# Kernel tuning notes

Measured on AMD Instinct MI355X. Metric: run time of the kernel, lower is better.

The kernel has to match this reference:

```python
import jax, jax.numpy as jnp
import numpy as np

KNN_K = 5  # nearest neighbors for local density
PATCH_GRID = 14  # hard-coded p1=p2=14 in rearrange


def _tokens(x):
    # b c (p1 h) (p2 w) -> b (p1 p2) (h w c)
    B, C, H, W = x.shape
    P = PATCH_GRID
    h, w = H // P, W // P
    t = x.reshape(B, C, P, h, P, w).transpose(0, 2, 4, 3, 5, 1)
    return t.reshape(B, P * P, h * w * C)


def _forward(x, len_keep):
    t = _tokens(x)
    B, N, Cf = t.shape
    # pairwise Euclidean distance (torch.cdist) scaled by sqrt(C)
    sq = jnp.sum(t * t, axis=-1)  # [B, N]
    d2 = sq[:, :, None] + sq[:, None, :] - 2.0 * jnp.einsum('bnc,bmc->bnm', t, t)
    dist = jnp.sqrt(jnp.maximum(d2, 0.0)) / jnp.sqrt(jnp.asarray(Cf, dist_dtype := t.dtype))
    # k-NN local density
    neg_vals, _ = jax.lax.top_k(-dist, KNN_K)  # k smallest distances
    dist_nearest = -neg_vals  # [B, N, k]
    density = jnp.exp(-jnp.mean(dist_nearest ** 2, axis=-1))  # [B, N]
    kd = jax.random.fold_in(jax.random.key(1), 0)
    density = density + jax.random.uniform(kd, density.shape, dtype=density.dtype) * 1e-6
    # distance to nearest higher-density point (masked min reduction)
    maskf = (density[:, None, :] > density[:, :, None]).astype(dist.dtype)  # [B, N, N]
    dist_max = jnp.max(dist.reshape(B, -1), axis=-1)[:, None, None]
    dmin = jnp.min(dist * maskf + dist_max * (1.0 - maskf), axis=-1)  # [B, N]
    score = dmin * density
    # pick cluster centers: top len_keep scores
    _, index_down = jax.lax.top_k(score, len_keep)  # [B, K]
    # assign each token to nearest center
    dm_down = jnp.take_along_axis(dist, index_down[:, :, None], axis=1)  # [B, K, N]
    idx_cluster = jnp.argmin(dm_down, axis=1)  # [B, N]
    # force centers to their own cluster id
    idx_cluster = idx_cluster.at[jnp.arange(B)[:, None], index_down].set(
        jnp.arange(len_keep)[None, :])
    # per-cluster counts (every cluster id 0..K-1 present since centers self-assign)
    counts = jnp.sum(jax.nn.one_hot(idx_cluster, len_keep, dtype=jnp.int32), axis=1)  # [B, K]
    idx_counts = jnp.cumsum(counts, axis=-1)
    # pick one representative token per cluster via noisy sort
    kn = jax.random.fold_in(jax.random.key(1), 1)
    noise = jax.random.uniform(kn, (B, N), dtype=dist.dtype)
    order = jnp.argsort(idx_cluster.astype(dist.dtype) + noise, axis=-1)
    idx = jnp.take_along_axis(order, idx_counts - 1, axis=1)  # [B, K]
    return idx


def setup_inputs() -> dict:
    key = jax.random.key(0)
    x = jax.random.normal(key, (256, 3, 224, 224), dtype=jnp.float32)
    return {"x": x, "len_keep": 49}


def reference(x, len_keep):
    return _forward(x, len_keep)
```

## Files before the change

### kernel.cpp

```cpp
#include <hip/hip_runtime.h>
#include <stdint.h>

#define NTOK 196
#define KCL 49
#define IMG 224
#define IMG2 (224*224)
#define KB 64
#define LDP 68

typedef double f64x4 __attribute__((ext_vector_type(4)));

__host__ __device__ __forceinline__ void tf2x32(uint32_t k0, uint32_t k1,
    uint32_t x0, uint32_t x1, uint32_t* o0, uint32_t* o1) {
  uint32_t ks2 = k0 ^ k1 ^ 0x1BD11BDAu;
#define TFR(r) { x0 += x1; x1 = (x1 << r) | (x1 >> (32 - r)); x1 ^= x0; }
  x0 += k0; x1 += k1;
  TFR(13) TFR(15) TFR(26) TFR(6)
  x0 += k1; x1 += ks2 + 1u;
  TFR(17) TFR(29) TFR(16) TFR(24)
  x0 += ks2; x1 += k0 + 2u;
  TFR(13) TFR(15) TFR(26) TFR(6)
  x0 += k0; x1 += k1 + 3u;
  TFR(17) TFR(29) TFR(16) TFR(24)
  x0 += k1; x1 += ks2 + 4u;
  TFR(13) TFR(15) TFR(26) TFR(6)
  x0 += ks2; x1 += k0 + 5u;
#undef TFR
  *o0 = x0; *o1 = x1;
}

__device__ __forceinline__ float jax_uniform(uint32_t k0, uint32_t k1, uint32_t j) {
  uint32_t o0, o1;
  tf2x32(k0, k1, 0u, j, &o0, &o1);
  uint32_t bits = o0 ^ o1;
  return __uint_as_float((bits >> 9) | 0x3f800000u) - 1.0f;
}

__global__ void __launch_bounds__(256) k_sq(const float* __restrict__ x,
                                            double* __restrict__ sq, int B) {
  int wave = blockIdx.x * 4 + (threadIdx.x >> 6);
  int lane = threadIdx.x & 63;
  if (wave >= B * NTOK) return;
  int b = wave / NTOK, n = wave % NTOK;
  int p1 = n / 14, p2 = n % 14;
  const float* xb = x + (size_t)b * 3 * IMG2;
  int rowbase = (p1 * 16) * IMG + p2 * 16;
  double acc = 0.0;
#pragma unroll
  for (int q = 0; q < 12; ++q) {
    int f = lane + q * 64;
    int c = f >> 8, h = (f >> 4) & 15, w = f & 15;
    float v = xb[c * IMG2 + rowbase + h * IMG + w];
    acc += (double)v * (double)v;
  }
#pragma unroll
  for (int off = 32; off; off >>= 1) acc += __shfl_down(acc, off);
  if (lane == 0) sq[wave] = acc;
}

__global__ void __launch_bounds__(256) k_dist_mfma(const float* __restrict__ x,
    const double* __restrict__ sq, double* __restrict__ dist,
    unsigned long long* __restrict__ dmax) {
  int bid = blockIdx.x;
  int xcd = bid & 7;
  int s = bid >> 3;
  int b = xcd + 8 * (s / 28);
  int t = s % 28;
  int ti = 0, rem = t, rl = 7;
  while (rem >= rl) { rem -= rl; rl--; ti++; }
  int tj = ti + rem;
  int n0b = ti * 32, m0b = tj * 32;
  int tid = threadIdx.x;

  __shared__ __align__(16) float As[32][LDP];
  __shared__ __align__(16) float Bs[32][LDP];
  __shared__ int rbN[32], rbM[32];
  __shared__ double prsh[3];
  __shared__ int okf;

  if (tid < 32) {
    int n = n0b + tid; n = n < NTOK ? n : NTOK - 1;
    rbN[tid] = (n / 14) * 16 * IMG + (n % 14) * 16;
  } else if (tid < 64) {
    int m = m0b + (tid - 32); m = m < NTOK ? m : NTOK - 1;
    rbM[tid - 32] = (m / 14) * 16 * IMG + (m % 14) * 16;
  }
  __syncthreads();

  const float* xb = x + (size_t)b * 3 * IMG2;
  int srow = tid >> 3;
  int sfo  = (tid & 7) * 8;
  int rN = rbN[srow], rM = rbM[srow];
  int lane = tid & 63;
  int wid  = tid >> 6;
  int wi = wid >> 1, wj = wid & 1;
  int aq = lane >> 4;
  const float* Ap = &As[0][0];
  const float* Bp = &Bs[0][0];
  int abase = (wi * 16 + (lane & 15)) * LDP + aq;
  int bbase = (wj * 16 + (lane & 15)) * LDP + aq;

#define LOADT(d0,d1,d2,d3,kc) { int f0 = (kc) + sfo;                         \
    int c_ = f0 >> 8, h_ = (f0 >> 4) & 15, w_ = f0 & 15;                     \
    const float* p_ = xb + c_ * IMG2 + h_ * IMG + w_;                        \
    d0 = *(const float4*)(p_ + rN); d1 = *(const float4*)(p_ + rN + 4);      \
    d2 = *(const float4*)(p_ + rM); d3 = *(const float4*)(p_ + rM + 4); }

  f64x4 acc = {0.0, 0.0, 0.0, 0.0};
  f64x4 acc0 = {0.0, 0.0, 0.0, 0.0};
  float4 ca0, ca1, cb0, cb1;
  LOADT(ca0, ca1, cb0, cb1, 0)

#pragma unroll
  for (int tt = 0; tt < 12; ++tt) {
    __syncthreads();
    *(float4*)&As[srow][sfo]     = ca0;
    *(float4*)&As[srow][sfo + 4] = ca1;
    *(float4*)&Bs[srow][sfo]     = cb0;
    *(float4*)&Bs[srow][sfo + 4] = cb1;
    __syncthreads();
    float4 na0, na1, nb0, nb1;
    if (tt < 11) LOADT(na0, na1, nb0, nb1, (tt + 1) * KB)
#pragma unroll
    for (int k = 0; k < KB; k += 4) {
      double av = (double)Ap[abase + k];
      double bv = (double)Bp[bbase + k];
      acc = __builtin_amdgcn_mfma_f64_16x16x4f64(av, bv, acc, 0, 0, 0);
    }
    if (tt == 0) {
      if (wid == 0) {
        double q0 = (double)As[0][lane] * (double)Bs[0][lane];
        double q1 = (double)As[1][lane] * (double)Bs[0][lane];
        double q2 = (double)As[4][lane] * (double)Bs[0][lane];
#pragma unroll
        for (int off = 32; off; off >>= 1) {
          q0 += __shfl_down(q0, off);
          q1 += __shfl_down(q1, off);
          q2 += __shfl_down(q2, off);
        }
        if (lane == 0) { prsh[0] = q0; prsh[1] = q1; prsh[2] = q2; }
      }
      acc0 = acc;
    }
    ca0 = na0; ca1 = na1; cb0 = nb0; cb1 = nb1;
  }
#undef LOADT

  if (tid == 0) {
    double tol = 1e-9 * (1.0 + fabs(prsh[0]));
    int ok0  = fabs(prsh[0] - acc0[0]) <= tol;
    int okP1 = ok0 && (fabs(prsh[1] - acc0[1]) <= tol);
    int okP2 = ok0 && (fabs(prsh[2] - acc0[1]) <= tol);
    okf = okP1 ? 1 : (okP2 ? 2 : 0);
  }
  __syncthreads();
  int mode = okf;

  double (*Dt)[33] = (double(*)[33])(&As[0][0]);

  if (mode) {
#pragma unroll
    for (int i = 0; i < 4; ++i) {
      int lr = (mode == 1) ? (aq * 4 + i) : (aq + 4 * i);
      Dt[wi * 16 + lr][wj * 16 + (lane & 15)] = acc[i];
    }
  } else {
    double s00 = 0, s01 = 0, s10 = 0, s11 = 0;
    int ty2 = tid >> 4, tx2 = tid & 15;
    for (int kc = 0; kc < 768; kc += KB) {
      int f0 = kc + sfo;
      int c_ = f0 >> 8, h_ = (f0 >> 4) & 15, w_ = f0 & 15;
      const float* p_ = xb + c_ * IMG2 + h_ * IMG + w_;
      float4 la0 = *(const float4*)(p_ + rN), la1 = *(const float4*)(p_ + rN + 4);
      float4 lb0 = *(const float4*)(p_ + rM), lb1 = *(const float4*)(p_ + rM + 4);
      __syncthreads();
      *(float4*)&As[srow][sfo]     = la0;
      *(float4*)&As[srow][sfo + 4] = la1;
      *(float4*)&Bs[srow][sfo]     = lb0;
      *(float4*)&Bs[srow][sfo + 4] = lb1;
      __syncthreads();
      for (int j = 0; j < KB; ++j) {
        double a0 = (double)As[ty2][j], a1 = (double)As[ty2 + 16][j];
        double b0 = (double)Bs[tx2][j], b1 = (double)Bs[tx2 + 16][j];
        s00 += a0 * b0; s01 += a0 * b1; s10 += a1 * b0; s11 += a1 * b1;
      }
    }
    __syncthreads();
    Dt[ty2][tx2] = s00;       Dt[ty2][tx2 + 16] = s01;
    Dt[ty2 + 16][tx2] = s10;  Dt[ty2 + 16][tx2 + 16] = s11;
  }
  __syncthreads();

  const double* sqb = sq + b * NTOK;
  const double SQ768 = sqrt(768.0);
  int lr2 = tid >> 3, lc0 = (tid & 7) * 4;
  double dv[4];
  double lmax = 0.0;
#pragma unroll
  for (int j = 0; j < 4; ++j) {
    int n = n0b + lr2, m = m0b + lc0 + j;
    int nn = n < NTOK ? n : NTOK - 1, mm = m < NTOK ? m : NTOK - 1;
    double d2 = sqb[nn] + sqb[mm] - 2.0 * Dt[lr2][lc0 + j];
    double d = sqrt(d2 > 0.0 ? d2 : 0.0) / SQ768;
    dv[j] = d;
    Dt[lr2][lc0 + j] = d;
    lmax = lmax > d ? lmax : d;
  }
  double* red = (double*)(&Bs[0][0]);
  red[tid] = lmax;
  __syncthreads();
  for (int st = 128; st; st >>= 1) {
    if (tid < st) { double o = red[tid + st]; if (o > red[tid]) red[tid] = o; }
    __syncthreads();
  }
  if (tid == 0) atomicMax(&dmax[b], (unsigned long long)__double_as_longlong(red[0]));

  double* Db = dist + (size_t)b * NTOK * NTOK;
  {
    int n = n0b + lr2, m0 = m0b + lc0;
    if (n < NTOK && m0 < NTOK) {
      if (m0 + 3 < NTOK) {
        f64x4 v = {dv[0], dv[1], dv[2], dv[3]};
        *(f64x4*)(Db + (size_t)n * NTOK + m0) = v;
      } else {
#pragma unroll
        for (int j = 0; j < 4; ++j)
          if (m0 + j < NTOK) Db[(size_t)n * NTOK + m0 + j] = dv[j];
      }
    }
  }
  if (ti != tj) {
    int m = m0b + lr2, n0 = n0b + lc0;
    if (m < NTOK && n0 < NTOK) {
      if (n0 + 3 < NTOK) {
        f64x4 v = {Dt[lc0][lr2], Dt[lc0 + 1][lr2], Dt[lc0 + 2][lr2], Dt[lc0 + 3][lr2]};
        *(f64x4*)(Db + (size_t)m * NTOK + n0) = v;
      } else {
#pragma unroll
        for (int j = 0; j < 4; ++j)
          if (n0 + j < NTOK) Db[(size_t)m * NTOK + n0 + j] = Dt[lc0 + j][lr2];
      }
    }
  }
}

__global__ void __launch_bounds__(256) k_cluster(const double* __restrict__ dist,
    const unsigned long long* __restrict__ dmax, int* __restrict__ out,
    uint32_t kd0, uint32_t kd1, uint32_t kn0, uint32_t kn1, int B) {
  int b = blockIdx.x;
  int tid = threadIdx.x;
  int lane = tid & 63, wid = tid >> 6;
  const double* Db = dist + (size_t)b * NTOK * NTOK;
  __shared__ double dens[NTOK];
  __shared__ double score[NTOK];
  __shared__ int center[KCL];
  __shared__ short center_of[NTOK];
  __shared__ unsigned long long bkey[KCL];
  double dmaxv = __longlong_as_double((long long)dmax[b]);

  if (tid < NTOK) {
    double nb0 = 1e300, nb1 = 1e300, nb2 = 1e300, nb3 = 1e300, nb4 = 1e300;
    for (int m = 0; m < NTOK; ++m) {
      double v = Db[(size_t)m * NTOK + tid];
      if (v < nb4) {
        nb4 = v;
        if (nb4 < nb3) { double t = nb3; nb3 = nb4; nb4 = t;
          if (nb3 < nb2) { t = nb2; nb2 = nb3; nb3 = t;
            if (nb2 < nb1) { t = nb1; nb1 = nb2; nb2 = t;
              if (nb1 < nb0) { t = nb0; nb0 = nb1; nb1 = t; } } } }
      }
    }
    double acc = nb0 * nb0 + nb1 * nb1 + nb2 * nb2 + nb3 * nb3 + nb4 * nb4;
    double mean = acc / 5.0;
    double d = exp(-mean);
    double u = (double)jax_uniform(kd0, kd1, (uint32_t)(b * NTOK + tid));
    dens[tid] = d + u * 1e-6;
  }
  __syncthreads();

  if (tid < NTOK) {
    double dn = dens[tid];
    double v = dmaxv;
    for (int m = 0; m < NTOK; ++m) {
      double r = Db[(size_t)m * NTOK + tid];
      if (dens[m] > dn && r < v) v = r;
    }
    score[tid] = v * dn;
  }
  __syncthreads();

  if (wid == 0) {
    double s0 = (lane < NTOK) ? score[lane] : -1e300;
    double s1 = score[lane + 64];
    double s2 = score[lane + 128];
    double s3 = (lane + 192 < NTOK) ? score[lane + 192] : -1e300;
    for (int k = 0; k < KCL; ++k) {
      double mv = s0; int mi = lane;
      if (s1 > mv) { mv = s1; mi = lane + 64; }
      if (s2 > mv) { mv = s2; mi = lane + 128; }
      if (s3 > mv) { mv = s3; mi = lane + 192; }
#pragma unroll
      for (int off = 32; off; off >>= 1) {
        double ov = __shfl_down(mv, off); int oi = __shfl_down(mi, off);
        if (ov > mv || (ov == mv && oi < mi)) { mv = ov; mi = oi; }
      }
      mi = __shfl(mi, 0);
      if (lane == 0) center[k] = mi;
      if (mi == lane) s0 = -1e300;
      else if (mi == lane + 64) s1 = -1e300;
      else if (mi == lane + 128) s2 = -1e300;
      else if (mi == lane + 192) s3 = -1e300;
    }
  }
  __syncthreads();

  if (tid < NTOK) center_of[tid] = -1;
  __syncthreads();
  if (tid < KCL) { center_of[center[tid]] = (short)tid; bkey[tid] = 0ULL; }
  __syncthreads();
  int mycl = 0;
  if (tid < NTOK) {
    double best = 1e300; int bk = 0;
    for (int k = 0; k < KCL; ++k) {
      double d = Db[(size_t)center[k] * NTOK + tid];
      if (d < best) { best = d; bk = k; }
    }
    short co = center_of[tid];
    if (co >= 0) bk = co;
    mycl = bk;
  }
  __syncthreads();

  if (tid < NTOK) {
    float u = jax_uniform(kn0, kn1, (uint32_t)(b * NTOK + tid));
    float keyf = (float)mycl + u;
    unsigned long long key =
        ((unsigned long long)__float_as_uint(keyf) << 8) | (unsigned)tid;
    atomicMax(&bkey[mycl], key);
  }
  __syncthreads();
  if (tid < KCL) out[b * KCL + tid] = (int)(bkey[tid] & 0xFFu);
}

extern "C" void kernel_launch(void* const* d_in, const int* in_sizes, int n_in,
                              void* d_out, int out_size, void* d_ws, size_t ws_size,
                              hipStream_t stream) {
  const float* x = (const float*)d_in[0];
  int B = in_sizes[0] / (3 * IMG2);
  double* dist = (double*)d_ws;
  size_t distBytes = (size_t)B * NTOK * NTOK * sizeof(double);
  double* sq = (double*)((char*)d_ws + distBytes);
  unsigned long long* dmax =
      (unsigned long long*)((char*)sq + (size_t)B * NTOK * sizeof(double));
  int* out = (int*)d_out;

  uint32_t kd0, kd1, kn0, kn1;
  tf2x32(0u, 1u, 0u, 0u, &kd0, &kd1);
  tf2x32(0u, 1u, 0u, 1u, &kn0, &kn1);

  hipMemsetAsync(dmax, 0, B * sizeof(unsigned long long), stream);
  int totalTok = B * NTOK;
  k_sq<<<dim3((totalTok + 3) / 4), dim3(256), 0, stream>>>(x, sq, B);
  k_dist_mfma<<<dim3(8 * 32 * 28), dim3(256), 0, stream>>>(x, sq, dist, dmax);
  k_cluster<<<dim3(B), dim3(256), 0, stream>>>(dist, dmax, out, kd0, kd1, kn0, kn1, B);
}
```

Before: 364.2 us.

## Fuse squared-norm computation into distance kernel and split cluster scans across 512 threads

Removes the separate k_sq kernel by accumulating per-token squared norms inside the distance kernel from the tiles it already loads, then reducing them in shared memory. This saves one launch and a re-read of the input, at the cost of extra FP64 FMAs and shared memory in the distance kernel. The cluster kernel now uses 512 threads, and each token's kNN and masked-min column scans are split into two halves that are merged through shared memory. This doubles parallelism over the per-batch serial dependency chain.

```diff
diff --git a/kernel.cpp b/kernel.cpp
--- a/kernel.cpp
+++ b/kernel.cpp
@@ -36,31 +36,8 @@
   return __uint_as_float((bits >> 9) | 0x3f800000u) - 1.0f;
 }
 
-__global__ void __launch_bounds__(256) k_sq(const float* __restrict__ x,
-                                            double* __restrict__ sq, int B) {
-  int wave = blockIdx.x * 4 + (threadIdx.x >> 6);
-  int lane = threadIdx.x & 63;
-  if (wave >= B * NTOK) return;
-  int b = wave / NTOK, n = wave % NTOK;
-  int p1 = n / 14, p2 = n % 14;
-  const float* xb = x + (size_t)b * 3 * IMG2;
-  int rowbase = (p1 * 16) * IMG + p2 * 16;
-  double acc = 0.0;
-#pragma unroll
-  for (int q = 0; q < 12; ++q) {
-    int f = lane + q * 64;
-    int c = f >> 8, h = (f >> 4) & 15, w = f & 15;
-    float v = xb[c * IMG2 + rowbase + h * IMG + w];
-    acc += (double)v * (double)v;
-  }
-#pragma unroll
-  for (int off = 32; off; off >>= 1) acc += __shfl_down(acc, off);
-  if (lane == 0) sq[wave] = acc;
-}
-
 __global__ void __launch_bounds__(256) k_dist_mfma(const float* __restrict__ x,
-    const double* __restrict__ sq, double* __restrict__ dist,
-    unsigned long long* __restrict__ dmax) {
+    double* __restrict__ dist, unsigned long long* __restrict__ dmax) {
   int bid = blockIdx.x;
   int xcd = bid & 7;
   int s = bid >> 3;
@@ -77,6 +54,8 @@
   __shared__ int rbN[32], rbM[32];
   __shared__ double prsh[3];
   __shared__ int okf;
+  __shared__ double sqpA[32][8], sqpB[32][8];
+  __shared__ double sqN[32], sqM[32];
 
   if (tid < 32) {
     int n = n0b + tid; n = n < NTOK ? n : NTOK - 1;
@@ -108,6 +87,7 @@
 
   f64x4 acc = {0.0, 0.0, 0.0, 0.0};
   f64x4 acc0 = {0.0, 0.0, 0.0, 0.0};
+  double psqA = 0.0, psqB = 0.0;
   float4 ca0, ca1, cb0, cb1;
   LOADT(ca0, ca1, cb0, cb1, 0)
 
@@ -118,6 +98,14 @@
     *(float4*)&As[srow][sfo + 4] = ca1;
     *(float4*)&Bs[srow][sfo]     = cb0;
     *(float4*)&Bs[srow][sfo + 4] = cb1;
+    psqA += (double)ca0.x * ca0.x; psqA += (double)ca0.y * ca0.y;
+    psqA += (double)ca0.z * ca0.z; psqA += (double)ca0.w * ca0.w;
+    psqA += (double)ca1.x * ca1.x; psqA += (double)ca1.y * ca1.y;
+    psqA += (double)ca1.z * ca1.z; psqA += (double)ca1.w * ca1.w;
+    psqB += (double)cb0.x * cb0.x; psqB += (double)cb0.y * cb0.y;
+    psqB += (double)cb0.z * cb0.z; psqB += (double)cb0.w * cb0.w;
+    psqB += (double)cb1.x * cb1.x; psqB += (double)cb1.y * cb1.y;
+    psqB += (double)cb1.z * cb1.z; psqB += (double)cb1.w * cb1.w;
     __syncthreads();
     float4 na0, na1, nb0, nb1;
     if (tt < 11) LOADT(na0, na1, nb0, nb1, (tt + 1) * KB)
@@ -146,6 +134,8 @@
   }
 #undef LOADT
 
+  sqpA[srow][tid & 7] = psqA;
+  sqpB[srow][tid & 7] = psqB;
   if (tid == 0) {
     double tol = 1e-9 * (1.0 + fabs(prsh[0]));
     int ok0  = fabs(prsh[0] - acc0[0]) <= tol;
@@ -189,23 +179,32 @@
     Dt[ty2][tx2] = s00;       Dt[ty2][tx2 + 16] = s01;
     Dt[ty2 + 16][tx2] = s10;  Dt[ty2 + 16][tx2 + 16] = s11;
   }
-  __syncthreads();
-
-  const double* sqb = sq + b * NTOK;
+  if (tid < 32) {
+    double a = sqpA[tid][0];
+#pragma unroll
+    for (int j = 1; j < 8; ++j) a += sqpA[tid][j];
+    sqN[tid] = a;
+  } else if (tid < 64) {
+    double a = sqpB[tid - 32][0];
+#pragma unroll
+    for (int j = 1; j < 8; ++j) a += sqpB[tid - 32][j];
+    sqM[tid - 32] = a;
+  }
+  __syncthreads();
+
   const double SQ768 = sqrt(768.0);
   int lr2 = tid >> 3, lc0 = (tid & 7) * 4;
   double dv[4];
   double lmax = 0.0;
 #pragma unroll
   for (int j = 0; j < 4; ++j) {
-    int n = n0b + lr2, m = m0b + lc0 + j;
-    int nn = n < NTOK ? n : NTOK - 1, mm = m < NTOK ? m : NTOK - 1;
-    double d2 = sqb[nn] + sqb[mm] - 2.0 * Dt[lr2][lc0 + j];
+    double d2 = sqN[lr2] + sqM[lc0 + j] - 2.0 * Dt[lr2][lc0 + j];
     double d = sqrt(d2 > 0.0 ? d2 : 0.0) / SQ768;
     dv[j] = d;
-    Dt[lr2][lc0 + j] = d;
     lmax = lmax > d ? lmax : d;
   }
+#pragma unroll
+  for (int j = 0; j < 4; ++j) Dt[lr2][lc0 + j] = dv[j];
   double* red = (double*)(&Bs[0][0]);
   red[tid] = lmax;
   __syncthreads();
@@ -244,13 +243,14 @@
   }
 }
 
-__global__ void __launch_bounds__(256) k_cluster(const double* __restrict__ dist,
+__global__ void __launch_bounds__(512) k_cluster2(const double* __restrict__ dist,
     const unsigned long long* __restrict__ dmax, int* __restrict__ out,
     uint32_t kd0, uint32_t kd1, uint32_t kn0, uint32_t kn1, int B) {
   int b = blockIdx.x;
   int tid = threadIdx.x;
   int lane = tid & 63, wid = tid >> 6;
   const double* Db = dist + (size_t)b * NTOK * NTOK;
+  __shared__ double nbsh[NTOK * 5];
   __shared__ double dens[NTOK];
   __shared__ double score[NTOK];
   __shared__ int center[KCL];
@@ -258,34 +258,62 @@
   __shared__ unsigned long long bkey[KCL];
   double dmaxv = __longlong_as_double((long long)dmax[b]);
 
-  if (tid < NTOK) {
-    double nb0 = 1e300, nb1 = 1e300, nb2 = 1e300, nb3 = 1e300, nb4 = 1e300;
-    for (int m = 0; m < NTOK; ++m) {
-      double v = Db[(size_t)m * NTOK + tid];
+  int t = (tid < NTOK) ? tid : tid - NTOK;
+  int half = (tid < NTOK) ? 0 : 1;
+  bool act = tid < 2 * NTOK;
+  int m0 = half ? 98 : 0, m1 = half ? NTOK : 98;
+
+  double nb0 = 1e300, nb1 = 1e300, nb2 = 1e300, nb3 = 1e300, nb4 = 1e300;
+  if (act) {
+    for (int m = m0; m < m1; ++m) {
+      double v = Db[(size_t)m * NTOK + t];
       if (v < nb4) {
         nb4 = v;
-        if (nb4 < nb3) { double t = nb3; nb3 = nb4; nb4 = t;
-          if (nb3 < nb2) { t = nb2; nb2 = nb3; nb3 = t;
-            if (nb2 < nb1) { t = nb1; nb1 = nb2; nb2 = t;
-              if (nb1 < nb0) { t = nb0; nb0 = nb1; nb1 = t; } } } }
-      }
-    }
-    double acc = nb0 * nb0 + nb1 * nb1 + nb2 * nb2 + nb3 * nb3 + nb4 * nb4;
-    double mean = acc / 5.0;
-    double d = exp(-mean);
-    double u = (double)jax_uniform(kd0, kd1, (uint32_t)(b * NTOK + tid));
-    dens[tid] = d + u * 1e-6;
-  }
-  __syncthreads();
-
+        if (nb4 < nb3) { double w = nb3; nb3 = nb4; nb4 = w;
+          if (nb3 < nb2) { w = nb2; nb2 = nb3; nb3 = w;
+            if (nb2 < nb1) { w = nb1; nb1 = nb2; nb2 = w;
+              if (nb1 < nb0) { w = nb0; nb0 = nb1; nb1 = w; } } } }
+      }
+    }
+    if (half) {
+      nbsh[t * 5 + 0] = nb0; nbsh[t * 5 + 1] = nb1; nbsh[t * 5 + 2] = nb2;
+      nbsh[t * 5 + 3] = nb3; nbsh[t * 5 + 4] = nb4;
+    }
+  }
+  __syncthreads();
   if (tid < NTOK) {
-    double dn = dens[tid];
-    double v = dmaxv;
-    for (int m = 0; m < NTOK; ++m) {
-      double r = Db[(size_t)m * NTOK + tid];
-      if (dens[m] > dn && r < v) v = r;
-    }
-    score[tid] = v * dn;
+    double ax = nb0, a1 = nb1, a2 = nb2, a3 = nb3, a4 = nb4;
+    double bx = nbsh[t * 5 + 0], b1 = nbsh[t * 5 + 1], b2 = nbsh[t * 5 + 2],
+           b3 = nbsh[t * 5 + 3], b4 = nbsh[t * 5 + 4];
+    double acc = 0.0;
+#pragma unroll
+    for (int p = 0; p < 5; ++p) {
+      double v;
+      if (ax <= bx) { v = ax; ax = a1; a1 = a2; a2 = a3; a3 = a4; a4 = 1e300; }
+      else          { v = bx; bx = b1; b1 = b2; b2 = b3; b3 = b4; b4 = 1e300; }
+      acc += v * v;
+    }
+    double d = exp(-(acc / 5.0));
+    double u = (double)jax_uniform(kd0, kd1, (uint32_t)(b * NTOK + t));
+    dens[t] = d + u * 1e-6;
+  }
+  __syncthreads();
+
+  double vloc = dmaxv;
+  if (act) {
+    double dn = dens[t];
+    for (int m = m0; m < m1; ++m) {
+      double r = Db[(size_t)m * NTOK + t];
+      if (dens[m] > dn && r < vloc) vloc = r;
+    }
+  }
+  __syncthreads();
+  if (act && half) nbsh[t] = vloc;
+  __syncthreads();
+  if (tid < NTOK) {
+    double v2 = nbsh[t];
+    double v = vloc < v2 ? vloc : v2;
+    score[t] = v * dens[t];
   }
   __syncthreads();
 
@@ -349,9 +377,7 @@
   int B = in_sizes[0] / (3 * IMG2);
   double* dist = (double*)d_ws;
   size_t distBytes = (size_t)B * NTOK * NTOK * sizeof(double);
-  double* sq = (double*)((char*)d_ws + distBytes);
-  unsigned long long* dmax =
-      (unsigned long long*)((char*)sq + (size_t)B * NTOK * sizeof(double));
+  unsigned long long* dmax = (unsigned long long*)((char*)d_ws + distBytes);
   int* out = (int*)d_out;
 
   uint32_t kd0, kd1, kn0, kn1;
@@ -359,8 +385,6 @@
   tf2x32(0u, 1u, 0u, 1u, &kn0, &kn1);
 
   hipMemsetAsync(dmax, 0, B * sizeof(unsigned long long), stream);
-  int totalTok = B * NTOK;
-  k_sq<<<dim3((totalTok + 3) / 4), dim3(256), 0, stream>>>(x, sq, B);
-  k_dist_mfma<<<dim3(8 * 32 * 28), dim3(256), 0, stream>>>(x, sq, dist, dmax);
-  k_cluster<<<dim3(B), dim3(256), 0, stream>>>(dist, dmax, out, kd0, kd1, kn0, kn1, B);
-}
+  k_dist_mfma<<<dim3(8 * 32 * 28), dim3(256), 0, stream>>>(x, dist, dmax);
+  k_cluster2<<<dim3(B), dim3(512), 0, stream>>>(dist, dmax, out, kd0, kd1, kn0, kn1, B);
+}
```

Result: no change. 363.2 us (-0.3%).

## Split k-NN and masked-min column scans across two thread halves in cluster kernel

Applied to the files above, without the earlier changes.

The cluster kernel now launches 512 threads per batch, so each token's column is scanned by two threads, each covering half of the rows with two interleaved independent chains. Partial top-5 lists and partial minima are merged through shared memory. The goal is more memory-level parallelism and shorter serial loops in what was a latency-bound per-batch kernel. The cost is extra syncs and shared memory, plus possible register pressure under the 512 launch bound. A small reorder of the LDS store in the distance kernel is also included.

```diff
diff --git a/kernel.cpp b/kernel.cpp
--- a/kernel.cpp
+++ b/kernel.cpp
@@ -203,9 +203,10 @@
     double d2 = sqb[nn] + sqb[mm] - 2.0 * Dt[lr2][lc0 + j];
     double d = sqrt(d2 > 0.0 ? d2 : 0.0) / SQ768;
     dv[j] = d;
-    Dt[lr2][lc0 + j] = d;
     lmax = lmax > d ? lmax : d;
   }
+#pragma unroll
+  for (int j = 0; j < 4; ++j) Dt[lr2][lc0 + j] = dv[j];
   double* red = (double*)(&Bs[0][0]);
   red[tid] = lmax;
   __syncthreads();
@@ -244,13 +245,21 @@
   }
 }
 
-__global__ void __launch_bounds__(256) k_cluster(const double* __restrict__ dist,
+#define INS5(n0_,n1_,n2_,n3_,n4_,v_) {                                        \
+  if ((v_) < n4_) { n4_ = (v_);                                               \
+    if (n4_ < n3_) { double w_ = n3_; n3_ = n4_; n4_ = w_;                    \
+      if (n3_ < n2_) { w_ = n2_; n2_ = n3_; n3_ = w_;                         \
+        if (n2_ < n1_) { w_ = n1_; n1_ = n2_; n2_ = w_;                       \
+          if (n1_ < n0_) { w_ = n0_; n0_ = n1_; n1_ = w_; } } } } } }
+
+__global__ void __launch_bounds__(512) k_cluster2(const double* __restrict__ dist,
     const unsigned long long* __restrict__ dmax, int* __restrict__ out,
     uint32_t kd0, uint32_t kd1, uint32_t kn0, uint32_t kn1, int B) {
   int b = blockIdx.x;
   int tid = threadIdx.x;
   int lane = tid & 63, wid = tid >> 6;
   const double* Db = dist + (size_t)b * NTOK * NTOK;
+  __shared__ double nbsh[NTOK * 5];
   __shared__ double dens[NTOK];
   __shared__ double score[NTOK];
   __shared__ int center[KCL];
@@ -258,34 +267,75 @@
   __shared__ unsigned long long bkey[KCL];
   double dmaxv = __longlong_as_double((long long)dmax[b]);
 
+  int t = (tid < NTOK) ? tid : tid - NTOK;
+  int half = (tid < NTOK) ? 0 : 1;
+  bool act = tid < 2 * NTOK;
+  int m0 = half ? 98 : 0;
+
+  double pa0 = 1e300, pa1 = 1e300, pa2 = 1e300, pa3 = 1e300, pa4 = 1e300;
+  double qa0 = 1e300, qa1 = 1e300, qa2 = 1e300, qa3 = 1e300, qa4 = 1e300;
+  if (act) {
+    const double* base = Db + t;
+    for (int i = 0; i < 49; ++i) {
+      double v1 = base[(size_t)(m0 + i) * NTOK];
+      double v2 = base[(size_t)(m0 + 49 + i) * NTOK];
+      INS5(pa0, pa1, pa2, pa3, pa4, v1)
+      INS5(qa0, qa1, qa2, qa3, qa4, v2)
+    }
+  }
+  double nb[5];
+  {
+    double ax = pa0, a1 = pa1, a2 = pa2, a3 = pa3, a4 = pa4;
+    double bx = qa0, b1 = qa1, b2 = qa2, b3 = qa3, b4 = qa4;
+#pragma unroll
+    for (int p = 0; p < 5; ++p) {
+      if (ax <= bx) { nb[p] = ax; ax = a1; a1 = a2; a2 = a3; a3 = a4; a4 = 1e300; }
+      else          { nb[p] = bx; bx = b1; b1 = b2; b2 = b3; b3 = b4; b4 = 1e300; }
+    }
+  }
+  if (act && half) {
+    nbsh[t * 5 + 0] = nb[0]; nbsh[t * 5 + 1] = nb[1]; nbsh[t * 5 + 2] = nb[2];
+    nbsh[t * 5 + 3] = nb[3]; nbsh[t * 5 + 4] = nb[4];
+  }
+  __syncthreads();
   if (tid < NTOK) {
-    double nb0 = 1e300, nb1 = 1e300, nb2 = 1e300, nb3 = 1e300, nb4 = 1e300;
-    for (int m = 0; m < NTOK; ++m) {
-      double v = Db[(size_t)m * NTOK + tid];
-      if (v < nb4) {
-        nb4 = v;
-        if (nb4 < nb3) { double t = nb3; nb3 = nb4; nb4 = t;
-          if (nb3 < nb2) { t = nb2; nb2 = nb3; nb3 = t;
-            if (nb2 < nb1) { t = nb1; nb1 = nb2; nb2 = t;
-              if (nb1 < nb0) { t = nb0; nb0 = nb1; nb1 = t; } } } }
-      }
-    }
-    double acc = nb0 * nb0 + nb1 * nb1 + nb2 * nb2 + nb3 * nb3 + nb4 * nb4;
-    double mean = acc / 5.0;
-    double d = exp(-mean);
-    double u = (double)jax_uniform(kd0, kd1, (uint32_t)(b * NTOK + tid));
-    dens[tid] = d + u * 1e-6;
-  }
-  __syncthreads();
-
+    double ax = nb[0], a1 = nb[1], a2 = nb[2], a3 = nb[3], a4 = nb[4];
+    double bx = nbsh[t * 5 + 0], b1 = nbsh[t * 5 + 1], b2 = nbsh[t * 5 + 2],
+           b3 = nbsh[t * 5 + 3], b4 = nbsh[t * 5 + 4];
+    double acc = 0.0;
+#pragma unroll
+    for (int p = 0; p < 5; ++p) {
+      double v;
+      if (ax <= bx) { v = ax; ax = a1; a1 = a2; a2 = a3; a3 = a4; a4 = 1e300; }
+      else          { v = bx; bx = b1; b1 = b2; b2 = b3; b3 = b4; b4 = 1e300; }
+      acc += v * v;
+    }
+    double d = exp(-(acc / 5.0));
+    double u = (double)jax_uniform(kd0, kd1, (uint32_t)(b * NTOK + t));
+    dens[t] = d + u * 1e-6;
+  }
+  __syncthreads();
+
+  double vloc = dmaxv;
+  if (act) {
+    double dn = dens[t];
+    const double* base = Db + t;
+    double v1 = dmaxv, v2 = dmaxv;
+    for (int i = 0; i < 49; ++i) {
+      double r1 = base[(size_t)(m0 + i) * NTOK];
+      double r2 = base[(size_t)(m0 + 49 + i) * NTOK];
+      if (dens[m0 + i] > dn && r1 < v1) v1 = r1;
+      if (dens[m0 + 49 + i] > dn && r2 < v2) v2 = r2;
+    }
+    vloc = v1 < v2 ? v1 : v2;
+  }
+  __syncthreads();
+  if (act && half) nbsh[t] = vloc;
+  __syncthreads();
   if (tid < NTOK) {
-    double dn = dens[tid];
-    double v = dmaxv;
-    for (int m = 0; m < NTOK; ++m) {
-      double r = Db[(size_t)m * NTOK + tid];
-      if (dens[m] > dn && r < v) v = r;
-    }
-    score[tid] = v * dn;
+    double v2 = nbsh[t];
+    double v = vloc < v2 ? vloc : v2;
+    score[t] = v * dens[t];
   }
   __syncthreads();
 
@@ -362,5 +412,5 @@
   int totalTok = B * NTOK;
   k_sq<<<dim3((totalTok + 3) / 4), dim3(256), 0, stream>>>(x, sq, B);
   k_dist_mfma<<<dim3(8 * 32 * 28), dim3(256), 0, stream>>>(x, sq, dist, dmax);
-  k_cluster<<<dim3(B), dim3(256), 0, stream>>>(dist, dmax, out, kd0, kd1, kn0, kn1, B);
-}
+  k_cluster2<<<dim3(B), dim3(512), 0, stream>>>(dist, dmax, out, kd0, kd1, kn0, kn1, B);
+}
```

Measured after the change: 319.1 us. -12.4%, faster.
